# Kernel tuning notes

Hardware: AMD Instinct MI355X
Metric: run time of the kernel (lower is better)

Reference implementation:

```python
import jax, jax.numpy as jnp
import numpy as np

ALPHA = 0.01
BETA = 1.0
PW_EPS = 1e-9   # eps inside pairwise_cross_entropy (function default)
UC_EPS = 1e-8   # eps inside uniform_cross_entropy


def setup_inputs() -> dict:
    key = jax.random.key(0)
    noises = jax.random.normal(key, (12, 4096, 16), dtype=jnp.float32)
    return {"noises": noises}


def reference(noises):
    layers, N, D = noises.shape
    p = jax.nn.softmax(noises, axis=-1)                      # [L, N, D]
    log_q = jnp.log(p + PW_EPS)                              # [L, N, D]
    # pairwise CE[l, i, j] = sum_d p[l,i,d] * log_q[l,j,d] == P @ log_Q^T
    ce = jnp.einsum('lnd,lmd->lnm', p, log_q)                # [L, N, N]
    diag_sum = jnp.einsum('lnn->', ce)
    aux_loss_1 = (ce.sum() - diag_sum) / (2.0 * layers)
    # uniform cross entropy on per-layer mean routing distribution
    pm = p.mean(axis=1)                                      # [L, D]
    pm = pm / pm.sum(axis=1, keepdims=True)
    aux_loss_2 = (-jnp.sum(jnp.log(pm + UC_EPS), axis=1) / D).mean()
    return ALPHA * (BETA * aux_loss_1 + aux_loss_2)
```

## Files before the change

kernel.cpp:

```cpp
#include <hip/hip_runtime.h>
#include <math.h>

#define LAYERS 12
#define NROWS  4096
#define DDIM   16
#define BLOCK  64
#define NBLK   ((LAYERS * NROWS) / BLOCK)
#define BLK_PER_LAYER (NROWS / BLOCK)
#define PART   33
#define PBLK2  256

__device__ __forceinline__ float wave_red6(float v) {
    #pragma unroll
    for (int off = 32; off > 0; off >>= 1)
        v += __shfl_xor(v, off, 64);
    return v;
}

__device__ __forceinline__ float red16(const float* v, int lane) {
    const bool b5 = lane & 32, b4 = lane & 16, b3 = lane & 8, b2 = lane & 4;
    float w8[8], w4[4], w2[2], w1;
    #pragma unroll
    for (int k = 0; k < 8; k++) {
        float t = b5 ? v[k] : v[k + 8];
        float o = __shfl_xor(t, 32, 64);
        w8[k] = (b5 ? v[k + 8] : v[k]) + o;
    }
    #pragma unroll
    for (int k = 0; k < 4; k++) {
        float t = b4 ? w8[k] : w8[k + 4];
        float o = __shfl_xor(t, 16, 64);
        w4[k] = (b4 ? w8[k + 4] : w8[k]) + o;
    }
    #pragma unroll
    for (int k = 0; k < 2; k++) {
        float t = b3 ? w4[k] : w4[k + 2];
        float o = __shfl_xor(t, 8, 64);
        w2[k] = (b3 ? w4[k + 2] : w4[k]) + o;
    }
    {
        float t = b2 ? w2[0] : w2[1];
        float o = __shfl_xor(t, 4, 64);
        w1 = (b2 ? w2[1] : w2[0]) + o;
    }
    w1 += __shfl_xor(w1, 2, 64);
    w1 += __shfl_xor(w1, 1, 64);
    return w1;
}

__global__ __launch_bounds__(BLOCK)
void moe_loss_pass1(const float* __restrict__ x, float* __restrict__ part) {
    const int lane = threadIdx.x;
    const int b    = blockIdx.x;

    const float4* x4 = (const float4*)x;
    const int r4 = (b * BLOCK + lane) * 4;
    float v[DDIM]; float4 a4;
    a4 = x4[r4 + 0]; v[0]  = a4.x; v[1]  = a4.y; v[2]  = a4.z; v[3]  = a4.w;
    a4 = x4[r4 + 1]; v[4]  = a4.x; v[5]  = a4.y; v[6]  = a4.z; v[7]  = a4.w;
    a4 = x4[r4 + 2]; v[8]  = a4.x; v[9]  = a4.y; v[10] = a4.z; v[11] = a4.w;
    a4 = x4[r4 + 3]; v[12] = a4.x; v[13] = a4.y; v[14] = a4.z; v[15] = a4.w;

    float m = v[0];
    #pragma unroll
    for (int d = 1; d < DDIM; d++) m = fmaxf(m, v[d]);
    float e[DDIM], s = 0.f;
    #pragma unroll
    for (int d = 0; d < DDIM; d++) { e[d] = __expf(v[d] - m); s += e[d]; }
    const float inv = __frcp_rn(s);

    float p[DDIM], lq[DDIM], diag = 0.f;
    #pragma unroll
    for (int d = 0; d < DDIM; d++) {
        p[d]  = e[d] * inv;
        lq[d] = __logf(p[d] + 1e-9f);
        diag += p[d] * lq[d];
    }

    const float sp = red16(p,  lane);
    const float sl = red16(lq, lane);
    const float dg = wave_red6(diag);

    const int g = lane >> 2, sub = lane & 3;
    if (sub == 0) part[g * NBLK + b] = sp;
    if (sub == 1) part[(DDIM + g) * NBLK + b] = sl;
    if (lane == 2) part[32 * NBLK + b] = dg;
}

__global__ __launch_bounds__(PBLK2)
void moe_loss_pass2(const float* __restrict__ part, float* __restrict__ out) {
    const int tid  = threadIdx.x;
    const int wave = tid >> 6;
    const int lane = tid & 63;

    __shared__ float sP[LAYERS][DDIM];
    const int l = tid >> 4, d = tid & 15;
    float a = 0.f, bq = 0.f;
    if (tid < LAYERS * DDIM) {
        const float4* pa = (const float4*)(part + d * NBLK + l * BLK_PER_LAYER);
        const float4* pb = (const float4*)(part + (DDIM + d) * NBLK + l * BLK_PER_LAYER);
        #pragma unroll
        for (int k = 0; k < BLK_PER_LAYER / 4; k++) {
            float4 va = pa[k]; a  += va.x + va.y + va.z + va.w;
            float4 vb = pb[k]; bq += vb.x + vb.y + vb.z + vb.w;
        }
        sP[l][d] = a;
    }
    __syncthreads();
    float ce_v = 0.f, lg_v = 0.f;
    if (tid < LAYERS * DDIM) {
        float S = 0.f;
        #pragma unroll
        for (int d2 = 0; d2 < DDIM; d2++) S += sP[l][d2];
        ce_v = a * bq;
        lg_v = __logf(a / S + 1e-8f);
    }
    const float* dgp = part + 32 * NBLK;
    const float dg_v = dgp[tid] + dgp[tid + 256] + dgp[tid + 512];

    __shared__ float red[3][PBLK2 / 64];
    const float r0 = wave_red6(ce_v), r1 = wave_red6(lg_v), r2 = wave_red6(dg_v);
    if (lane == 0) { red[0][wave] = r0; red[1][wave] = r1; red[2][wave] = r2; }
    __syncthreads();
    if (tid == 0) {
        const float ce = red[0][0] + red[0][1] + red[0][2] + red[0][3];
        const float lg = red[1][0] + red[1][1] + red[1][2] + red[1][3];
        const float dg = red[2][0] + red[2][1] + red[2][2] + red[2][3];
        const float aux1 = (ce - dg) / (2.0f * LAYERS);
        const float aux2 = (-lg / (float)DDIM) / (float)LAYERS;
        out[0] = 0.01f * (1.0f * aux1 + aux2);
    }
}

extern "C" void kernel_launch(void* const* d_in, const int* in_sizes, int n_in,
                              void* d_out, int out_size, void* d_ws, size_t ws_size,
                              hipStream_t stream) {
    const float* noises = (const float*)d_in[0];
    float* part = (float*)d_ws;
    float* out  = (float*)d_out;
    hipLaunchKernelGGL(moe_loss_pass1, dim3(NBLK), dim3(BLOCK), 0, stream, noises, part);
    hipLaunchKernelGGL(moe_loss_pass2, dim3(1), dim3(PBLK2), 0, stream, part, out);
}
```

Baseline: 59.45 us.

## Fuse both passes into one cooperative kernel with grid-wide sync

```diff
diff --git a/kernel.cpp b/kernel.cpp
--- a/kernel.cpp
+++ b/kernel.cpp
@@ -1,14 +1,16 @@
 #include <hip/hip_runtime.h>
+#include <hip/hip_cooperative_groups.h>
 #include <math.h>
+
+namespace cg = cooperative_groups;
 
 #define LAYERS 12
 #define NROWS  4096
 #define DDIM   16
-#define BLOCK  64
-#define NBLK   ((LAYERS * NROWS) / BLOCK)
-#define BLK_PER_LAYER (NROWS / BLOCK)
+#define BLOCK  256
+#define NBLK   192
+#define BPL    16
 #define PART   33
-#define PBLK2  256
 
 __device__ __forceinline__ float wave_red6(float v) {
     #pragma unroll
@@ -49,12 +51,15 @@
 }
 
 __global__ __launch_bounds__(BLOCK)
-void moe_loss_pass1(const float* __restrict__ x, float* __restrict__ part) {
-    const int lane = threadIdx.x;
+void moe_loss_fused(const float* __restrict__ x, float* __restrict__ part,
+                    float* __restrict__ out) {
+    const int tid  = threadIdx.x;
     const int b    = blockIdx.x;
+    const int wave = tid >> 6;
+    const int lane = tid & 63;
 
     const float4* x4 = (const float4*)x;
-    const int r4 = (b * BLOCK + lane) * 4;
+    const int r4 = (b * BLOCK + tid) * 4;
     float v[DDIM]; float4 a4;
     a4 = x4[r4 + 0]; v[0]  = a4.x; v[1]  = a4.y; v[2]  = a4.z; v[3]  = a4.w;
     a4 = x4[r4 + 1]; v[4]  = a4.x; v[5]  = a4.y; v[6]  = a4.z; v[7]  = a4.w;
@@ -81,26 +86,29 @@
     const float sl = red16(lq, lane);
     const float dg = wave_red6(diag);
 
-    const int g = lane >> 2, sub = lane & 3;
-    if (sub == 0) part[g * NBLK + b] = sp;
-    if (sub == 1) part[(DDIM + g) * NBLK + b] = sl;
-    if (lane == 2) part[32 * NBLK + b] = dg;
-}
+    __shared__ float lds[BLOCK / 64][PART];
+    {
+        const int g = lane >> 2, sub = lane & 3;
+        if (sub == 0) lds[wave][g] = sp;
+        if (sub == 1) lds[wave][DDIM + g] = sl;
+        if (lane == 2) lds[wave][32] = dg;
+    }
+    __syncthreads();
+    if (tid < PART)
+        part[tid * NBLK + b] = lds[0][tid] + lds[1][tid] + lds[2][tid] + lds[3][tid];
 
-__global__ __launch_bounds__(PBLK2)
-void moe_loss_pass2(const float* __restrict__ part, float* __restrict__ out) {
-    const int tid  = threadIdx.x;
-    const int wave = tid >> 6;
-    const int lane = tid & 63;
+    cg::this_grid().sync();
+
+    if (b != 0) return;
 
     __shared__ float sP[LAYERS][DDIM];
     const int l = tid >> 4, d = tid & 15;
     float a = 0.f, bq = 0.f;
     if (tid < LAYERS * DDIM) {
-        const float4* pa = (const float4*)(part + d * NBLK + l * BLK_PER_LAYER);
-        const float4* pb = (const float4*)(part + (DDIM + d) * NBLK + l * BLK_PER_LAYER);
+        const float4* pa = (const float4*)(part + d * NBLK + l * BPL);
+        const float4* pb = (const float4*)(part + (DDIM + d) * NBLK + l * BPL);
         #pragma unroll
-        for (int k = 0; k < BLK_PER_LAYER / 4; k++) {
+        for (int k = 0; k < BPL / 4; k++) {
             float4 va = pa[k]; a  += va.x + va.y + va.z + va.w;
             float4 vb = pb[k]; bq += vb.x + vb.y + vb.z + vb.w;
         }
@@ -115,10 +123,9 @@
         ce_v = a * bq;
         lg_v = __logf(a / S + 1e-8f);
     }
-    const float* dgp = part + 32 * NBLK;
-    const float dg_v = dgp[tid] + dgp[tid + 256] + dgp[tid + 512];
+    const float dg_v = (tid < NBLK) ? part[32 * NBLK + tid] : 0.f;
 
-    __shared__ float red[3][PBLK2 / 64];
+    __shared__ float red[3][BLOCK / 64];
     const float r0 = wave_red6(ce_v), r1 = wave_red6(lg_v), r2 = wave_red6(dg_v);
     if (lane == 0) { red[0][wave] = r0; red[1][wave] = r1; red[2][wave] = r2; }
     __syncthreads();
@@ -138,6 +145,7 @@
     const float* noises = (const float*)d_in[0];
     float* part = (float*)d_ws;
     float* out  = (float*)d_out;
-    hipLaunchKernelGGL(moe_loss_pass1, dim3(NBLK), dim3(BLOCK), 0, stream, noises, part);
-    hipLaunchKernelGGL(moe_loss_pass2, dim3(1), dim3(PBLK2), 0, stream, part, out);
+    void* args[] = { (void*)&noises, (void*)&part, (void*)&out };
+    hipLaunchCooperativeKernel((const void*)moe_loss_fused,
+                               dim3(NBLK), dim3(BLOCK), args, 0, stream);
 }
```

New measurement: 87.25 us. 46.7% more time.
